# Kernel tuning notes

Measured on AMD Instinct MI355X. Metric: run time of the kernel, lower is better.

Reference implementation:

```python
import jax, jax.numpy as jnp
import numpy as np

IGNORE_INDEX = -100
B, S, D, V = 4, 2048, 2048, 32000


def setup_inputs() -> dict:
    key = jax.random.key(0)
    k1, k2, k3, k4 = jax.random.split(key, 4)
    hidden = jax.random.normal(k1, (B, S, D), dtype=jnp.float32)
    targets = jax.random.randint(k2, (B, S), 0, V, dtype=jnp.int64)
    drop = jax.random.uniform(k3, (B, S)) < 0.1
    targets = jnp.where(drop, IGNORE_INDEX, targets)
    W = jax.random.normal(k4, (V, D), dtype=jnp.float32) * (D ** -0.5)
    return {"hidden": hidden, "targets": targets, "W": W}


def reference(hidden, targets, W):
    # hidden: [B, S, D], targets: [B, S] int, W: [V, D]
    mask = targets != IGNORE_INDEX                      # [B, S]
    total = mask.sum()
    # Linear projection to vocab, CE computed in fp32 (matches logits.float())
    logits = jnp.einsum('bsd,vd->bsv', hidden, W).astype(jnp.float32)  # [B, S, V]
    logp = jax.nn.log_softmax(logits, axis=-1)
    safe_t = jnp.where(mask, targets, 0)
    nll = -jnp.take_along_axis(logp, safe_t[..., None], axis=-1)[..., 0]  # [B, S]
    loss_sum = jnp.sum(jnp.where(mask, nll, 0.0))
    return loss_sum / total.astype(jnp.float32)
```

## Files before the change

kernel.cpp:

```cpp
#include <hip/hip_runtime.h>
#include <hip/hip_bf16.h>
#include <stdint.h>

#define IGNORE_INDEX (-100)

constexpr int M_ = 8192;
constexpr int K_ = 2048;
constexpr int N_ = 32000;

typedef __attribute__((ext_vector_type(4)))  float f32x4;
typedef __attribute__((ext_vector_type(16))) float f32x16;
typedef __attribute__((ext_vector_type(4)))  int   i32x4;
typedef __attribute__((ext_vector_type(8)))  int   i32x8;
typedef __attribute__((ext_vector_type(4)))  unsigned int u32x4;
typedef __attribute__((ext_vector_type(8)))  __bf16 bf16x8;

#define SCALE_A 8.0f
#define SCALE_W 1024.0f
#define INV_S   (1.0f / (8.0f * 1024.0f))

__device__ __forceinline__ unsigned pack_bf16(float f0, float f1) {
    unsigned u0 = __builtin_bit_cast(unsigned, f0) + 0x8000u;
    unsigned u1 = __builtin_bit_cast(unsigned, f1) + 0x8000u;
    return __builtin_amdgcn_perm(u1, u0, 0x07060302u);
}
__device__ __forceinline__ u32x4 pack8(f32x4 lo, f32x4 hi) {
    u32x4 r;
    r[0] = pack_bf16(lo[0], lo[1]);
    r[1] = pack_bf16(lo[2], lo[3]);
    r[2] = pack_bf16(hi[0], hi[1]);
    r[3] = pack_bf16(hi[2], hi[3]);
    return r;
}

__device__ __forceinline__ void gll16(const void* g, void* l) {
    __builtin_amdgcn_global_load_lds(
        (const __attribute__((address_space(1))) unsigned int*)g,
        (__attribute__((address_space(3))) unsigned int*)l, 16, 0, 0);
}

__global__ void init_acc(float* p, int n) {
    int i = blockIdx.x * 256 + threadIdx.x;
    if (i < n) p[i] = 0.0f;
}

__global__ __launch_bounds__(256) void convert_fp8(
    const float* __restrict__ in, unsigned int* __restrict__ out,
    float scale, int n8)
{
    int i = blockIdx.x * 256 + threadIdx.x;
    if (i < n8) {
        f32x4 lo = ((const f32x4*)in)[2 * i];
        f32x4 hi = ((const f32x4*)in)[2 * i + 1];
        int w0 = 0, w1 = 0;
        w0 = __builtin_amdgcn_cvt_pk_fp8_f32(lo[0] * scale, lo[1] * scale, w0, false);
        w0 = __builtin_amdgcn_cvt_pk_fp8_f32(lo[2] * scale, lo[3] * scale, w0, true);
        w1 = __builtin_amdgcn_cvt_pk_fp8_f32(hi[0] * scale, hi[1] * scale, w1, false);
        w1 = __builtin_amdgcn_cvt_pk_fp8_f32(hi[2] * scale, hi[3] * scale, w1, true);
        out[2 * i]     = (unsigned int)w0;
        out[2 * i + 1] = (unsigned int)w1;
    }
}


#define MFMA_SC(a, b, c) \
    __builtin_amdgcn_mfma_scale_f32_32x32x64_f8f6f4( \
        (a), (b), (c), 0, 0, 0, 0x7F7F7F7F, 0, 0x7F7F7F7F)

#define CAT8(lo, hi) (i32x8){(lo)[0], (lo)[1], (lo)[2], (lo)[3], \
                             (hi)[0], (hi)[1], (hi)[2], (hi)[3]}

#define LGKM0() do { \
    asm volatile("s_waitcnt lgkmcnt(0)" ::: "memory"); \
    __builtin_amdgcn_sched_barrier(0); \
} while (0)

template <bool STA, bool STB, int BVM>
__device__ __forceinline__ void ktile(
    const unsigned char* cA, const unsigned char* cB,
    unsigned char* nA, unsigned char* sB,
    const unsigned char* gAlo, const unsigned char* gAhi, int koffA,
    const unsigned char* gBlo, const unsigned char* gBhi, int koffB,
    int stoff, int aoffL, int aoffH, int boffL, int boffH,
    f32x16 (&acc)[4][2])
{
    i32x4 aL0 = *(const i32x4*)(cA + aoffL);
    i32x4 aH0 = *(const i32x4*)(cA + aoffH);
    i32x4 aL1 = *(const i32x4*)(cA + aoffL + 2048);
    i32x4 aH1 = *(const i32x4*)(cA + aoffH + 2048);
    i32x4 bL0 = *(const i32x4*)(cB + boffL);
    i32x4 bH0 = *(const i32x4*)(cB + boffH);
    if (STA) gll16(gAlo + koffA, nA + stoff);
    __builtin_amdgcn_s_barrier();
    LGKM0();
    i32x8 af0 = CAT8(aL0, aH0);
    i32x8 af1 = CAT8(aL1, aH1);
    i32x8 bf0 = CAT8(bL0, bH0);
    __builtin_amdgcn_s_setprio(1);
    acc[0][0] = MFMA_SC(af0, bf0, acc[0][0]);
    acc[1][0] = MFMA_SC(af1, bf0, acc[1][0]);
    __builtin_amdgcn_s_setprio(0);
    __builtin_amdgcn_s_barrier();

    i32x4 bL1 = *(const i32x4*)(cB + boffL + 2048);
    i32x4 bH1 = *(const i32x4*)(cB + boffH + 2048);
    if (STA) gll16(gAhi + koffA, nA + 8192 + stoff);
    __builtin_amdgcn_s_barrier();
    LGKM0();
    i32x8 bf1 = CAT8(bL1, bH1);
    __builtin_amdgcn_s_setprio(1);
    acc[0][1] = MFMA_SC(af0, bf1, acc[0][1]);
    acc[1][1] = MFMA_SC(af1, bf1, acc[1][1]);
    __builtin_amdgcn_s_setprio(0);
    __builtin_amdgcn_s_barrier();

    i32x4 aL2 = *(const i32x4*)(cA + aoffL + 4096);
    i32x4 aH2 = *(const i32x4*)(cA + aoffH + 4096);
    i32x4 aL3 = *(const i32x4*)(cA + aoffL + 6144);
    i32x4 aH3 = *(const i32x4*)(cA + aoffH + 6144);
    if (STB) gll16(gBlo + koffB, sB + stoff);
    __builtin_amdgcn_s_barrier();
    LGKM0();
    i32x8 af2 = CAT8(aL2, aH2);
    i32x8 af3 = CAT8(aL3, aH3);
    __builtin_amdgcn_s_setprio(1);
    acc[2][0] = MFMA_SC(af2, bf0, acc[2][0]);
    acc[3][0] = MFMA_SC(af3, bf0, acc[3][0]);
    __builtin_amdgcn_s_setprio(0);
    __builtin_amdgcn_s_barrier();

    if (STB) gll16(gBhi + koffB, sB + 8192 + stoff);
    __builtin_amdgcn_s_barrier();
    __builtin_amdgcn_s_setprio(1);
    acc[2][1] = MFMA_SC(af2, bf1, acc[2][1]);
    acc[3][1] = MFMA_SC(af3, bf1, acc[3][1]);
    __builtin_amdgcn_s_setprio(0);
    if constexpr (BVM == 0) {
        asm volatile("s_waitcnt vmcnt(0)" ::: "memory");
    } else if constexpr (BVM == 2) {
        asm volatile("s_waitcnt vmcnt(2)" ::: "memory");
    }
    __builtin_amdgcn_s_barrier();
}

__global__ __launch_bounds__(512, 2) void gemm_fp8(
    const unsigned char* __restrict__ A,
    const unsigned char* __restrict__ Wq,
    const int*   __restrict__ tgt,
    float* __restrict__ sumexp,
    float* __restrict__ tgtlogit)
{
    __shared__ __align__(16) unsigned char As[2][16384];
    __shared__ __align__(16) unsigned char Bs[2][16384];
    __shared__ int tg[256];

    const int tid = threadIdx.x;

    const int b  = blockIdx.x;
    const int b2 = (b & 7) * 500 + (b >> 3);
    const int mt = b2 & 31;
    const int nt = b2 >> 5;

    if (tid < 256) tg[tid] = tgt[mt * 256 + tid];

    const int wave = tid >> 6;
    const int lane = tid & 63;
    const int wm   = wave >> 2;
    const int wn   = wave & 3;

    const int srow = tid >> 2;
    const int spg  = (tid & 3) ^ ((srow >> 1) & 3);
    const unsigned char* gAlo = A  + (size_t)(mt * 256 + srow) * K_ + spg * 16;
    const unsigned char* gAhi = gAlo + (size_t)128 * K_;
    const unsigned char* gBlo = Wq + (size_t)(nt * 256 + srow) * K_ + spg * 16;
    const unsigned char* gBhi = gBlo + (size_t)128 * K_;
    const int stoff = wave * 1024;

    const int l31 = lane & 31;
    const int h   = lane >> 5;
    const int x   = (l31 >> 1) & 3;
    const int aoffL = (wm * 128 + l31) * 64 + ((2 * h)     ^ x) * 16;
    const int aoffH = (wm * 128 + l31) * 64 + ((2 * h + 1) ^ x) * 16;
    const int boffL = (wn * 64  + l31) * 64 + ((2 * h)     ^ x) * 16;
    const int boffH = (wn * 64  + l31) * 64 + ((2 * h + 1) ^ x) * 16;

    f32x16 acc[4][2];
#pragma unroll
    for (int m = 0; m < 4; m++)
#pragma unroll
        for (int n = 0; n < 2; n++)
#pragma unroll
            for (int r = 0; r < 16; r++) acc[m][n][r] = 0.f;

    gll16(gAlo,      As[0] + stoff);
    gll16(gAhi,      As[0] + 8192 + stoff);
    gll16(gBlo,      Bs[0] + stoff);
    gll16(gBhi,      Bs[0] + 8192 + stoff);
    gll16(gBlo + 64, Bs[1] + stoff);
    gll16(gBhi + 64, Bs[1] + 8192 + stoff);
    asm volatile("s_waitcnt vmcnt(2) lgkmcnt(0)" ::: "memory");
    __builtin_amdgcn_s_barrier();

#pragma unroll 1
    for (int it = 0; it < 15; ++it) {
        ktile<true, true, 2>(As[0], Bs[0], As[1], Bs[0],
                             gAlo, gAhi, 64, gBlo, gBhi, 128,
                             stoff, aoffL, aoffH, boffL, boffH, acc);
        ktile<true, true, 2>(As[1], Bs[1], As[0], Bs[1],
                             gAlo, gAhi, 128, gBlo, gBhi, 192,
                             stoff, aoffL, aoffH, boffL, boffH, acc);
        gAlo += 128; gAhi += 128; gBlo += 128; gBhi += 128;
    }
    ktile<true, false, 0>(As[0], Bs[0], As[1], Bs[0],
                          gAlo, gAhi, 64, gBlo, gBhi, 0,
                          stoff, aoffL, aoffH, boffL, boffH, acc);
    ktile<false, false, -1>(As[1], Bs[1], As[0], Bs[1],
                            gAlo, gAhi, 0, gBlo, gBhi, 0,
                            stoff, aoffL, aoffH, boffL, boffH, acc);

    const int c0 = nt * 256 + wn * 64 + l31;
#pragma unroll
    for (int ms = 0; ms < 4; ++ms) {
#pragma unroll
        for (int reg = 0; reg < 16; ++reg) {
            const int rbase = (reg & 3) + 8 * (reg >> 2) + 4 * h;
            const int lrow  = wm * 128 + ms * 32 + rbase;
            const int grow  = mt * 256 + lrow;
            const int t     = tg[lrow];
            float v0 = acc[ms][0][reg] * INV_S;
            float v1 = acc[ms][1][reg] * INV_S;
            if (t == c0)      tgtlogit[grow] = v0;
            if (t == c0 + 32) tgtlogit[grow] = v1;
            float rs = __expf(v0) + __expf(v1);
            rs += __shfl_xor(rs, 1);
            rs += __shfl_xor(rs, 2);
            rs += __shfl_xor(rs, 4);
            rs += __shfl_xor(rs, 8);
            rs += __shfl_xor(rs, 16);
            if (l31 == 0) atomicAdd(&sumexp[grow], rs);
        }
    }
}

constexpr int BMf = 128, BNf = 128;
constexpr int BKf = 32;
constexpr int LDA = BKf + 8;
__global__ __launch_bounds__(256) void gemm_fused_f32(
    const float* __restrict__ A,
    const float* __restrict__ W,
    const int*   __restrict__ tgt,
    float* __restrict__ sumexp,
    float* __restrict__ tgtlogit)
{
    __shared__ __bf16 As[BMf * LDA];
    __shared__ __bf16 Bs[BNf * LDA];
    __shared__ int    tg[BMf];

    const int tid = threadIdx.x;
    const int mt  = blockIdx.x;
    const int nt  = blockIdx.y;
    if (tid < BMf) tg[tid] = tgt[mt * BMf + tid];

    const int wave = tid >> 6, lane = tid & 63;
    const int wm = wave >> 1, wn = wave & 1;
    const int lquad = lane >> 4, lcol = lane & 15;
    const int srow = tid >> 2, scol = (tid & 3) * 8;

    const float* gA = A + (size_t)(mt * BMf + srow) * K_ + scol;
    const float* gB = W + (size_t)(nt * BNf + srow) * K_ + scol;
    const size_t rowstep = (size_t)64 * K_;

    f32x4 acc[4][4];
#pragma unroll
    for (int i = 0; i < 4; i++)
#pragma unroll
        for (int j = 0; j < 4; j++) acc[i][j] = (f32x4){0.f, 0.f, 0.f, 0.f};

    for (int kt = 0; kt < K_; kt += BKf) {
        f32x4 a0 = *(const f32x4*)(gA + kt);
        f32x4 a1 = *(const f32x4*)(gA + kt + 4);
        f32x4 a2 = *(const f32x4*)(gA + kt + rowstep);
        f32x4 a3 = *(const f32x4*)(gA + kt + rowstep + 4);
        f32x4 b0 = *(const f32x4*)(gB + kt);
        f32x4 b1 = *(const f32x4*)(gB + kt + 4);
        f32x4 b2 = *(const f32x4*)(gB + kt + rowstep);
        f32x4 b3 = *(const f32x4*)(gB + kt + rowstep + 4);
        __syncthreads();
        *(u32x4*)&As[srow * LDA + scol]        = pack8(a0, a1);
        *(u32x4*)&As[(srow + 64) * LDA + scol] = pack8(a2, a3);
        *(u32x4*)&Bs[srow * LDA + scol]        = pack8(b0, b1);
        *(u32x4*)&Bs[(srow + 64) * LDA + scol] = pack8(b2, b3);
        __syncthreads();
        bf16x8 af[4], bf[4];
#pragma unroll
        for (int f = 0; f < 4; f++) {
            af[f] = *(const bf16x8*)&As[(wm * 64 + f * 16 + lcol) * LDA + lquad * 8];
            bf[f] = *(const bf16x8*)&Bs[(wn * 64 + f * 16 + lcol) * LDA + lquad * 8];
        }
#pragma unroll
        for (int mf = 0; mf < 4; mf++)
#pragma unroll
            for (int nf = 0; nf < 4; nf++)
                acc[mf][nf] = __builtin_amdgcn_mfma_f32_16x16x32_bf16(af[mf], bf[nf], acc[mf][nf], 0, 0, 0);
    }
    const int colbase = nt * BNf + wn * 64;
#pragma unroll
    for (int mf = 0; mf < 4; mf++) {
#pragma unroll
        for (int r = 0; r < 4; r++) {
            const int lrow = wm * 64 + mf * 16 + lquad * 4 + r;
            const int grow = mt * BMf + lrow;
            const int t    = tg[lrow];
            float rs = 0.f;
#pragma unroll
            for (int nf = 0; nf < 4; nf++) {
                float v = acc[mf][nf][r];
                rs += __expf(v);
                if (t == colbase + nf * 16 + lcol) tgtlogit[grow] = v;
            }
            rs += __shfl_xor(rs, 1);
            rs += __shfl_xor(rs, 2);
            rs += __shfl_xor(rs, 4);
            rs += __shfl_xor(rs, 8);
            if (lcol == 0) atomicAdd(&sumexp[grow], rs);
        }
    }
}

__global__ __launch_bounds__(256) void finalize(
    const float* __restrict__ sumexp,
    const float* __restrict__ tgtlogit,
    const int*   __restrict__ tgt,
    float* __restrict__ out)
{
    float s = 0.f;
    int   c = 0;
    for (int i = threadIdx.x; i < M_; i += 256) {
        int t = tgt[i];
        if (t != IGNORE_INDEX) {
            s += __logf(sumexp[i]) - tgtlogit[i];
            c++;
        }
    }
#pragma unroll
    for (int o = 32; o; o >>= 1) {
        s += __shfl_down(s, o);
        c += __shfl_down(c, o);
    }
    __shared__ float ss[4];
    __shared__ int   cc[4];
    int w = threadIdx.x >> 6;
    if ((threadIdx.x & 63) == 0) { ss[w] = s; cc[w] = c; }
    __syncthreads();
    if (threadIdx.x == 0) {
        float st = ss[0] + ss[1] + ss[2] + ss[3];
        int   ct = cc[0] + cc[1] + cc[2] + cc[3];
        out[0] = st / (float)ct;
    }
}

extern "C" void kernel_launch(void* const* d_in, const int* in_sizes, int n_in,
                              void* d_out, int out_size, void* d_ws, size_t ws_size,
                              hipStream_t stream) {
    const float* hidden  = (const float*)d_in[0];
    const int*   targets = (const int*)d_in[1];
    const float* W       = (const float*)d_in[2];

    float* sumexp   = (float*)d_ws;
    float* tgtlogit = sumexp + M_;
    float* out      = (float*)d_out;

    unsigned char* Aq = (unsigned char*)d_ws + 2 * M_ * sizeof(float);
    unsigned char* Wq = Aq + (size_t)M_ * K_;
    const size_t need = 2 * M_ * sizeof(float) + (size_t)M_ * K_ + (size_t)N_ * K_;

    init_acc<<<(2 * M_ + 255) / 256, 256, 0, stream>>>(sumexp, 2 * M_);

    if (ws_size >= need) {
        const int a8 = M_ * K_ / 8;
        const int w8 = N_ * K_ / 8;
        convert_fp8<<<(a8 + 255) / 256, 256, 0, stream>>>(hidden, (unsigned int*)Aq, SCALE_A, a8);
        convert_fp8<<<(w8 + 255) / 256, 256, 0, stream>>>(W, (unsigned int*)Wq, SCALE_W, w8);
        gemm_fp8<<<(M_ / 256) * (N_ / 256), 512, 0, stream>>>(Aq, Wq, targets, sumexp, tgtlogit);
    } else {
        gemm_fused_f32<<<dim3(M_ / BMf, N_ / BNf), 256, 0, stream>>>(hidden, W, targets, sumexp, tgtlogit);
    }

    finalize<<<1, 256, 0, stream>>>(sumexp, tgtlogit, targets, out);
}
```

Before: 1.299 ms.

## Double K-tile depth to 128 in fp8 GEMM with dynamic LDS and new swizzle

The fp8 MFMA GEMM now stages 128-byte K slices per tile instead of 64, using 128 KB of dynamic shared memory, a new 8-way XOR swizzle, and two MFMAs per accumulator per phase. The goal is to halve the number of barrier-separated k-iterations and amortize synchronization and LDS-read overhead over more MFMA work. It also drops the block-index remapping that grouped tiles for L2 locality, and the larger LDS footprint may cut occupancy below the two blocks per CU requested in the launch bounds.

```diff
diff --git a/kernel.cpp b/kernel.cpp
--- a/kernel.cpp
+++ b/kernel.cpp
@@ -75,72 +75,112 @@
     __builtin_amdgcn_sched_barrier(0); \
 } while (0)
 
-template <bool STA, bool STB, int BVM>
+#define PREBAR() do { \
+    __builtin_amdgcn_sched_barrier(0); \
+    __builtin_amdgcn_s_barrier(); \
+} while (0)
+
+constexpr size_t CA = (size_t)64 * K_;
+
+template <bool S0, bool S1, int BVM>
 __device__ __forceinline__ void ktile(
     const unsigned char* cA, const unsigned char* cB,
-    unsigned char* nA, unsigned char* sB,
-    const unsigned char* gAlo, const unsigned char* gAhi, int koffA,
-    const unsigned char* gBlo, const unsigned char* gBhi, int koffB,
-    int stoff, int aoffL, int aoffH, int boffL, int boffH,
+    unsigned char* nA,
+    unsigned char* wA, unsigned char* wB,
+    const unsigned char* gA, const unsigned char* gB, int kt, int t16,
+    const int (&bA)[4][2], const int (&bB)[2][2],
     f32x16 (&acc)[4][2])
 {
-    i32x4 aL0 = *(const i32x4*)(cA + aoffL);
-    i32x4 aH0 = *(const i32x4*)(cA + aoffH);
-    i32x4 aL1 = *(const i32x4*)(cA + aoffL + 2048);
-    i32x4 aH1 = *(const i32x4*)(cA + aoffH + 2048);
-    i32x4 bL0 = *(const i32x4*)(cB + boffL);
-    i32x4 bH0 = *(const i32x4*)(cB + boffH);
-    if (STA) gll16(gAlo + koffA, nA + stoff);
-    __builtin_amdgcn_s_barrier();
+    i32x4 r0 = *(const i32x4*)(cA + bA[0][0]);
+    i32x4 r1 = *(const i32x4*)(cA + (bA[0][0] ^ 16));
+    i32x4 r2 = *(const i32x4*)(cA + bA[0][1]);
+    i32x4 r3 = *(const i32x4*)(cA + (bA[0][1] ^ 16));
+    i32x4 r4 = *(const i32x4*)(cA + bA[1][0]);
+    i32x4 r5 = *(const i32x4*)(cA + (bA[1][0] ^ 16));
+    i32x4 r6 = *(const i32x4*)(cA + bA[1][1]);
+    i32x4 r7 = *(const i32x4*)(cA + (bA[1][1] ^ 16));
+    i32x4 s0 = *(const i32x4*)(cB + bB[0][0]);
+    i32x4 s1 = *(const i32x4*)(cB + (bB[0][0] ^ 16));
+    i32x4 s2 = *(const i32x4*)(cB + bB[0][1]);
+    i32x4 s3 = *(const i32x4*)(cB + (bB[0][1] ^ 16));
+    if (S0) {
+        gll16(gA + 1 * CA + kt + 128, nA + 1 * 8192 + t16);
+        gll16(gA + 3 * CA + kt + 128, nA + 3 * 8192 + t16);
+    }
+    PREBAR();
     LGKM0();
-    i32x8 af0 = CAT8(aL0, aH0);
-    i32x8 af1 = CAT8(aL1, aH1);
-    i32x8 bf0 = CAT8(bL0, bH0);
+    i32x8 a00 = CAT8(r0, r1), a01 = CAT8(r2, r3);
+    i32x8 a10 = CAT8(r4, r5), a11 = CAT8(r6, r7);
+    i32x8 b00 = CAT8(s0, s1), b01 = CAT8(s2, s3);
     __builtin_amdgcn_s_setprio(1);
-    acc[0][0] = MFMA_SC(af0, bf0, acc[0][0]);
-    acc[1][0] = MFMA_SC(af1, bf0, acc[1][0]);
+    acc[0][0] = MFMA_SC(a00, b00, acc[0][0]);
+    acc[0][0] = MFMA_SC(a01, b01, acc[0][0]);
+    acc[1][0] = MFMA_SC(a10, b00, acc[1][0]);
+    acc[1][0] = MFMA_SC(a11, b01, acc[1][0]);
     __builtin_amdgcn_s_setprio(0);
     __builtin_amdgcn_s_barrier();
 
-    i32x4 bL1 = *(const i32x4*)(cB + boffL + 2048);
-    i32x4 bH1 = *(const i32x4*)(cB + boffH + 2048);
-    if (STA) gll16(gAhi + koffA, nA + 8192 + stoff);
-    __builtin_amdgcn_s_barrier();
+    i32x4 u0 = *(const i32x4*)(cB + bB[1][0]);
+    i32x4 u1 = *(const i32x4*)(cB + (bB[1][0] ^ 16));
+    i32x4 u2 = *(const i32x4*)(cB + bB[1][1]);
+    i32x4 u3 = *(const i32x4*)(cB + (bB[1][1] ^ 16));
+    if (S1) {
+        gll16(gA + 0 * CA + kt + 256, wA + 0 * 8192 + t16);
+        gll16(gA + 2 * CA + kt + 256, wA + 2 * 8192 + t16);
+    }
+    PREBAR();
     LGKM0();
-    i32x8 bf1 = CAT8(bL1, bH1);
+    i32x8 b10 = CAT8(u0, u1), b11 = CAT8(u2, u3);
     __builtin_amdgcn_s_setprio(1);
-    acc[0][1] = MFMA_SC(af0, bf1, acc[0][1]);
-    acc[1][1] = MFMA_SC(af1, bf1, acc[1][1]);
+    acc[0][1] = MFMA_SC(a00, b10, acc[0][1]);
+    acc[0][1] = MFMA_SC(a01, b11, acc[0][1]);
+    acc[1][1] = MFMA_SC(a10, b10, acc[1][1]);
+    acc[1][1] = MFMA_SC(a11, b11, acc[1][1]);
     __builtin_amdgcn_s_setprio(0);
     __builtin_amdgcn_s_barrier();
 
-    i32x4 aL2 = *(const i32x4*)(cA + aoffL + 4096);
-    i32x4 aH2 = *(const i32x4*)(cA + aoffH + 4096);
-    i32x4 aL3 = *(const i32x4*)(cA + aoffL + 6144);
-    i32x4 aH3 = *(const i32x4*)(cA + aoffH + 6144);
-    if (STB) gll16(gBlo + koffB, sB + stoff);
-    __builtin_amdgcn_s_barrier();
+    i32x4 v0 = *(const i32x4*)(cA + bA[2][0]);
+    i32x4 v1 = *(const i32x4*)(cA + (bA[2][0] ^ 16));
+    i32x4 v2 = *(const i32x4*)(cA + bA[2][1]);
+    i32x4 v3 = *(const i32x4*)(cA + (bA[2][1] ^ 16));
+    i32x4 v4 = *(const i32x4*)(cA + bA[3][0]);
+    i32x4 v5 = *(const i32x4*)(cA + (bA[3][0] ^ 16));
+    i32x4 v6 = *(const i32x4*)(cA + bA[3][1]);
+    i32x4 v7 = *(const i32x4*)(cA + (bA[3][1] ^ 16));
+    if (S1) {
+        gll16(gB + 0 * CA + kt + 256, wB + 0 * 8192 + t16);
+        gll16(gB + 1 * CA + kt + 256, wB + 1 * 8192 + t16);
+    }
+    PREBAR();
     LGKM0();
-    i32x8 af2 = CAT8(aL2, aH2);
-    i32x8 af3 = CAT8(aL3, aH3);
+    i32x8 a20 = CAT8(v0, v1), a21 = CAT8(v2, v3);
+    i32x8 a30 = CAT8(v4, v5), a31 = CAT8(v6, v7);
     __builtin_amdgcn_s_setprio(1);
-    acc[2][0] = MFMA_SC(af2, bf0, acc[2][0]);
-    acc[3][0] = MFMA_SC(af3, bf0, acc[3][0]);
+    acc[2][1] = MFMA_SC(a20, b10, acc[2][1]);
+    acc[2][1] = MFMA_SC(a21, b11, acc[2][1]);
+    acc[3][1] = MFMA_SC(a30, b10, acc[3][1]);
+    acc[3][1] = MFMA_SC(a31, b11, acc[3][1]);
     __builtin_amdgcn_s_setprio(0);
     __builtin_amdgcn_s_barrier();
 
-    if (STB) gll16(gBhi + koffB, sB + 8192 + stoff);
-    __builtin_amdgcn_s_barrier();
+    if (S1) {
+        gll16(gB + 2 * CA + kt + 256, wB + 2 * 8192 + t16);
+        gll16(gB + 3 * CA + kt + 256, wB + 3 * 8192 + t16);
+    }
+    PREBAR();
     __builtin_amdgcn_s_setprio(1);
-    acc[2][1] = MFMA_SC(af2, bf1, acc[2][1]);
-    acc[3][1] = MFMA_SC(af3, bf1, acc[3][1]);
+    acc[2][0] = MFMA_SC(a20, b00, acc[2][0]);
+    acc[2][0] = MFMA_SC(a21, b01, acc[2][0]);
+    acc[3][0] = MFMA_SC(a30, b00, acc[3][0]);
+    acc[3][0] = MFMA_SC(a31, b01, acc[3][0]);
     __builtin_amdgcn_s_setprio(0);
-    if constexpr (BVM == 0) {
+    if constexpr (BVM == 6) {
+        asm volatile("s_waitcnt vmcnt(6)" ::: "memory");
+        __builtin_amdgcn_s_barrier();
+    } else if constexpr (BVM == 0) {
         asm volatile("s_waitcnt vmcnt(0)" ::: "memory");
-    } else if constexpr (BVM == 2) {
-        asm volatile("s_waitcnt vmcnt(2)" ::: "memory");
-    }
-    __builtin_amdgcn_s_barrier();
+        __builtin_amdgcn_s_barrier();
+    }
 }
 
 __global__ __launch_bounds__(512, 2) void gemm_fp8(
@@ -150,16 +190,17 @@
     float* __restrict__ sumexp,
     float* __restrict__ tgtlogit)
 {
-    __shared__ __align__(16) unsigned char As[2][16384];
-    __shared__ __align__(16) unsigned char Bs[2][16384];
-    __shared__ int tg[256];
+    extern __shared__ unsigned char smem[];
+    unsigned char* As0 = smem;
+    unsigned char* As1 = smem + 32768;
+    unsigned char* Bs0 = smem + 65536;
+    unsigned char* Bs1 = smem + 98304;
+    int* tg = (int*)(smem + 131072);
 
     const int tid = threadIdx.x;
-
-    const int b  = blockIdx.x;
-    const int b2 = (b & 7) * 500 + (b >> 3);
-    const int mt = b2 & 31;
-    const int nt = b2 >> 5;
+    const int bid = blockIdx.x;
+    const int mt  = bid & 31;
+    const int nt  = bid >> 5;
 
     if (tid < 256) tg[tid] = tgt[mt * 256 + tid];
 
@@ -168,67 +209,77 @@
     const int wm   = wave >> 2;
     const int wn   = wave & 3;
 
-    const int srow = tid >> 2;
-    const int spg  = (tid & 3) ^ ((srow >> 1) & 3);
-    const unsigned char* gAlo = A  + (size_t)(mt * 256 + srow) * K_ + spg * 16;
-    const unsigned char* gAhi = gAlo + (size_t)128 * K_;
-    const unsigned char* gBlo = Wq + (size_t)(nt * 256 + srow) * K_ + spg * 16;
-    const unsigned char* gBhi = gBlo + (size_t)128 * K_;
-    const int stoff = wave * 1024;
+    const int sw16 = ((tid & 7) ^ ((tid >> 5) & 7)) << 4;
+    const unsigned char* gA = A  + (size_t)(mt * 256 + (tid >> 3)) * K_ + sw16;
+    const unsigned char* gB = Wq + (size_t)(nt * 256 + (tid >> 3)) * K_ + sw16;
+    const int t16 = tid << 4;
 
     const int l31 = lane & 31;
     const int h   = lane >> 5;
-    const int x   = (l31 >> 1) & 3;
-    const int aoffL = (wm * 128 + l31) * 64 + ((2 * h)     ^ x) * 16;
-    const int aoffH = (wm * 128 + l31) * 64 + ((2 * h + 1) ^ x) * 16;
-    const int boffL = (wn * 64  + l31) * 64 + ((2 * h)     ^ x) * 16;
-    const int boffH = (wn * 64  + l31) * 64 + ((2 * h + 1) ^ x) * 16;
+    int bA[4][2], bB[2][2];
+#pragma unroll
+    for (int m = 0; m < 4; ++m) {
+        const int row = wm * 128 + m * 32 + l31;
+        const int xa  = ((row >> 2) & 7) << 4;
+#pragma unroll
+        for (int ks = 0; ks < 2; ++ks)
+            bA[m][ks] = row * 128 + (((ks << 6) | (h << 5)) ^ xa);
+    }
+#pragma unroll
+    for (int n = 0; n < 2; ++n) {
+        const int row = wn * 64 + n * 32 + l31;
+        const int xb  = ((row >> 2) & 7) << 4;
+#pragma unroll
+        for (int ks = 0; ks < 2; ++ks)
+            bB[n][ks] = row * 128 + (((ks << 6) | (h << 5)) ^ xb);
+    }
 
     f32x16 acc[4][2];
 #pragma unroll
-    for (int m = 0; m < 4; m++)
-#pragma unroll
-        for (int n = 0; n < 2; n++)
-#pragma unroll
-            for (int r = 0; r < 16; r++) acc[m][n][r] = 0.f;
-
-    gll16(gAlo,      As[0] + stoff);
-    gll16(gAhi,      As[0] + 8192 + stoff);
-    gll16(gBlo,      Bs[0] + stoff);
-    gll16(gBhi,      Bs[0] + 8192 + stoff);
-    gll16(gBlo + 64, Bs[1] + stoff);
-    gll16(gBhi + 64, Bs[1] + 8192 + stoff);
-    asm volatile("s_waitcnt vmcnt(2) lgkmcnt(0)" ::: "memory");
+    for (int m = 0; m < 4; ++m)
+#pragma unroll
+        for (int n = 0; n < 2; ++n)
+#pragma unroll
+            for (int r = 0; r < 16; ++r) acc[m][n][r] = 0.f;
+
+#pragma unroll
+    for (int c = 0; c < 4; ++c) gll16(gA + c * CA, As0 + c * 8192 + t16);
+#pragma unroll
+    for (int c = 0; c < 4; ++c) gll16(gB + c * CA, Bs0 + c * 8192 + t16);
+    gll16(gA + 0 * CA + 128, As1 + 0 * 8192 + t16);
+    gll16(gA + 2 * CA + 128, As1 + 2 * 8192 + t16);
+    gll16(gB + 0 * CA + 128, Bs1 + 0 * 8192 + t16);
+    gll16(gB + 1 * CA + 128, Bs1 + 1 * 8192 + t16);
+    gll16(gB + 2 * CA + 128, Bs1 + 2 * 8192 + t16);
+    gll16(gB + 3 * CA + 128, Bs1 + 3 * 8192 + t16);
+    asm volatile("s_waitcnt vmcnt(6) lgkmcnt(0)" ::: "memory");
     __builtin_amdgcn_s_barrier();
 
+    int kt = 0;
 #pragma unroll 1
-    for (int it = 0; it < 15; ++it) {
-        ktile<true, true, 2>(As[0], Bs[0], As[1], Bs[0],
-                             gAlo, gAhi, 64, gBlo, gBhi, 128,
-                             stoff, aoffL, aoffH, boffL, boffH, acc);
-        ktile<true, true, 2>(As[1], Bs[1], As[0], Bs[1],
-                             gAlo, gAhi, 128, gBlo, gBhi, 192,
-                             stoff, aoffL, aoffH, boffL, boffH, acc);
-        gAlo += 128; gAhi += 128; gBlo += 128; gBhi += 128;
-    }
-    ktile<true, false, 0>(As[0], Bs[0], As[1], Bs[0],
-                          gAlo, gAhi, 64, gBlo, gBhi, 0,
-                          stoff, aoffL, aoffH, boffL, boffH, acc);
-    ktile<false, false, -1>(As[1], Bs[1], As[0], Bs[1],
-                            gAlo, gAhi, 0, gBlo, gBhi, 0,
-                            stoff, aoffL, aoffH, boffL, boffH, acc);
+    for (int it = 0; it < 7; ++it) {
+        ktile<true, true, 6>(As0, Bs0, As1, As0, Bs0,
+                             gA, gB, kt,       t16, bA, bB, acc);
+        ktile<true, true, 6>(As1, Bs1, As0, As1, Bs1,
+                             gA, gB, kt + 128, t16, bA, bB, acc);
+        kt += 256;
+    }
+    ktile<true, false, 0>(As0, Bs0, As1, As0, Bs0,
+                          gA, gB, 1792, t16, bA, bB, acc);
+    ktile<false, false, -1>(As1, Bs1, As0, As1, Bs1,
+                            gA, gB, 1920, t16, bA, bB, acc);
 
     const int c0 = nt * 256 + wn * 64 + l31;
 #pragma unroll
-    for (int ms = 0; ms < 4; ++ms) {
+    for (int m = 0; m < 4; ++m) {
 #pragma unroll
         for (int reg = 0; reg < 16; ++reg) {
             const int rbase = (reg & 3) + 8 * (reg >> 2) + 4 * h;
-            const int lrow  = wm * 128 + ms * 32 + rbase;
+            const int lrow  = wm * 128 + m * 32 + rbase;
             const int grow  = mt * 256 + lrow;
             const int t     = tg[lrow];
-            float v0 = acc[ms][0][reg] * INV_S;
-            float v1 = acc[ms][1][reg] * INV_S;
+            float v0 = acc[m][0][reg] * INV_S;
+            float v1 = acc[m][1][reg] * INV_S;
             if (t == c0)      tgtlogit[grow] = v0;
             if (t == c0 + 32) tgtlogit[grow] = v1;
             float rs = __expf(v0) + __expf(v1);
@@ -377,11 +428,18 @@
     init_acc<<<(2 * M_ + 255) / 256, 256, 0, stream>>>(sumexp, 2 * M_);
 
     if (ws_size >= need) {
+        static bool attr_set = false;
+        if (!attr_set) {
+            hipFuncSetAttribute(reinterpret_cast<const void*>(gemm_fp8),
+                                hipFuncAttributeMaxDynamicSharedMemorySize,
+                                132096);
+            attr_set = true;
+        }
         const int a8 = M_ * K_ / 8;
         const int w8 = N_ * K_ / 8;
         convert_fp8<<<(a8 + 255) / 256, 256, 0, stream>>>(hidden, (unsigned int*)Aq, SCALE_A, a8);
         convert_fp8<<<(w8 + 255) / 256, 256, 0, stream>>>(W, (unsigned int*)Wq, SCALE_W, w8);
-        gemm_fp8<<<(M_ / 256) * (N_ / 256), 512, 0, stream>>>(Aq, Wq, targets, sumexp, tgtlogit);
+        gemm_fp8<<<(M_ / 256) * (N_ / 256), 512, 132096, stream>>>(Aq, Wq, targets, sumexp, tgtlogit);
     } else {
         gemm_fused_f32<<<dim3(M_ / BMf, N_ / BNf), 256, 0, stream>>>(hidden, W, targets, sumexp, tgtlogit);
     }
```

Result: no change. 1.287 ms (-0.9%).
